# Kernel optimization log

Hardware: AMD Instinct MI355X
Metric: run time of the kernel (lower is better)

## Reference

```python
import jax, jax.numpy as jnp
import numpy as np

DIM = 512
K = 64          # num_clusters
GHOST = 1
ALPHA = 100.0
EPS = 1e-12


def _l2norm(v, axis):
    return v / jnp.maximum(jnp.linalg.norm(v, axis=axis, keepdims=True), EPS)


def setup_inputs() -> dict:
    key = jax.random.key(0)
    k_x, k_c = jax.random.split(key)
    x = jax.random.normal(k_x, (64, DIM, 32, 32), dtype=jnp.float32)
    # centroids ~ orthogonal init in torch; random normal rows, unit-ish scale
    centroids = jax.random.normal(k_c, (K + GHOST, DIM), dtype=jnp.float32) / np.sqrt(DIM)
    conv_w = 2.0 * ALPHA * centroids            # [K+g, C] (1x1 conv kernel squeezed)
    conv_b = -ALPHA * jnp.linalg.norm(centroids, axis=1)  # [K+g]
    return {"x": x, "centroids": centroids, "conv_w": conv_w, "conv_b": conv_b}


def reference(x, centroids, conv_w, conv_b):
    N, C, H, W = x.shape
    L = H * W
    # descriptor-wise L2 normalization over channel dim
    xn = _l2norm(x, axis=1)
    xf = xn.reshape(N, C, L)                                   # [N, C, L]
    # 1x1 conv == per-location matmul; softmax over clusters
    logits = jnp.einsum('kc,ncl->nkl', conv_w, xf) + conv_b[None, :, None]
    a = jax.nn.softmax(logits, axis=1)                         # [N, K+g, L]
    # vlad[n,k,c] = sum_l a[n,k,l]*(x[n,c,l]-cent[k,c])
    #            = (a @ x^T) - (sum_l a) * cent   -- avoids NxKxCxL tensor
    weighted = jnp.einsum('nkl,ncl->nkc', a, xf)               # [N, K+g, C]
    a_sum = jnp.sum(a, axis=-1)                                # [N, K+g]
    vlad = weighted - a_sum[:, :, None] * centroids[None]      # [N, K+g, C]
    vlad = vlad[:, :K, :]                                      # drop ghost clusters
    vlad = _l2norm(vlad, axis=2)                               # intra-normalization
    vlad = vlad.reshape(N, K * C)
    vlad = _l2norm(vlad, axis=1)                               # global L2
    return vlad
```

## Files before the change

### kernel.cpp

```cpp
#include <hip/hip_runtime.h>
#include <hip/hip_bf16.h>

#define C_DIM 512
#define L_DIM 1024
#define KK 64
#define KG 65
#define KP 80

using f32x4  = __attribute__((ext_vector_type(4))) float;
using bf16x8 = __attribute__((ext_vector_type(8))) short;

union U4 { uint4 u; bf16x8 b; };

__device__ __forceinline__ unsigned bfh(float x) { return __float_as_uint(x) >> 16; }
__device__ __forceinline__ float bfh_f(float x) { return __uint_as_float(__float_as_uint(x) & 0xFFFF0000u); }

__device__ __forceinline__ unsigned pack2(float a, float b) {
    return __builtin_amdgcn_perm(__float_as_uint(b), __float_as_uint(a), 0x07060302u);
}

__global__ void k_prep(const float* __restrict__ conv_w, const float* __restrict__ conv_b,
                       unsigned short* __restrict__ wpH, unsigned short* __restrict__ wpL,
                       float* __restrict__ wb)
{
    int ch = blockIdx.x;
    int kt = blockIdx.y;
    int t  = threadIdx.x;
    for (int p = 0; p < 2; ++p) {
        int idx = p * 256 + t;
        int lane = idx >> 3, j = idx & 7;
        int k = kt * 16 + (lane & 15);
        int c = ch * 32 + (lane >> 4) * 8 + j;
        float v = (k < KG) ? conv_w[k * C_DIM + c] : 0.f;
        unsigned h = bfh(v);
        float r = v - __uint_as_float(h << 16);
        int pos = ((ch * 5 + kt) << 9) + idx;
        wpH[pos] = (unsigned short)h;
        wpL[pos] = (unsigned short)bfh(r);
    }
    if (ch == 0 && kt == 0 && t < KP) wb[t] = (t < KG) ? conv_b[t] : -1e30f;
}

__global__ __launch_bounds__(256) void k_s1(
    const float* __restrict__ x, const unsigned short* __restrict__ wpH,
    const unsigned short* __restrict__ wpL, const float* __restrict__ wb,
    unsigned short* __restrict__ aPh, unsigned short* __restrict__ aPl,
    float* __restrict__ asum_part)
{
    const int lb = blockIdx.x, n = blockIdx.y;
    const int t = threadIdx.x, lane = t & 63, w = t >> 6;
    const int arow = lane & 15;
    const int agrp = lane >> 4;
    const int lw0 = lb * 128 + w * 32;

    const float* xbase = x + (size_t)n * C_DIM * L_DIM;

    f32x4 acc[5][2];
#pragma unroll
    for (int a = 0; a < 5; ++a)
#pragma unroll
        for (int b = 0; b < 2; ++b) acc[a][b] = (f32x4)0.f;
    float ss0 = 0.f, ss1 = 0.f;

    for (int ch = 0; ch < 16; ++ch) {
        const int c0 = ch * 32;
        float e0[8], e1[8];
#pragma unroll
        for (int j = 0; j < 8; ++j) {
            float2 v = *reinterpret_cast<const float2*>(
                &xbase[(size_t)(c0 + agrp * 8 + j) * L_DIM + lw0 + 2 * arow]);
            e0[j] = v.x;
            e1[j] = v.y;
        }
#pragma unroll
        for (int j = 0; j < 8; ++j) { ss0 += e0[j] * e0[j]; ss1 += e1[j] * e1[j]; }
        U4 bh[2], bl[2];
        bh[0].u.x = pack2(e0[0], e0[1]); bh[0].u.y = pack2(e0[2], e0[3]);
        bh[0].u.z = pack2(e0[4], e0[5]); bh[0].u.w = pack2(e0[6], e0[7]);
        bh[1].u.x = pack2(e1[0], e1[1]); bh[1].u.y = pack2(e1[2], e1[3]);
        bh[1].u.z = pack2(e1[4], e1[5]); bh[1].u.w = pack2(e1[6], e1[7]);
        float r0, r1, r2, r3;
        r0 = e0[0] - bfh_f(e0[0]); r1 = e0[1] - bfh_f(e0[1]);
        r2 = e0[2] - bfh_f(e0[2]); r3 = e0[3] - bfh_f(e0[3]);
        bl[0].u.x = pack2(r0, r1); bl[0].u.y = pack2(r2, r3);
        r0 = e0[4] - bfh_f(e0[4]); r1 = e0[5] - bfh_f(e0[5]);
        r2 = e0[6] - bfh_f(e0[6]); r3 = e0[7] - bfh_f(e0[7]);
        bl[0].u.z = pack2(r0, r1); bl[0].u.w = pack2(r2, r3);
        r0 = e1[0] - bfh_f(e1[0]); r1 = e1[1] - bfh_f(e1[1]);
        r2 = e1[2] - bfh_f(e1[2]); r3 = e1[3] - bfh_f(e1[3]);
        bl[1].u.x = pack2(r0, r1); bl[1].u.y = pack2(r2, r3);
        r0 = e1[4] - bfh_f(e1[4]); r1 = e1[5] - bfh_f(e1[5]);
        r2 = e1[6] - bfh_f(e1[6]); r3 = e1[7] - bfh_f(e1[7]);
        bl[1].u.z = pack2(r0, r1); bl[1].u.w = pack2(r2, r3);
        U4 ah[5], al[5];
#pragma unroll
        for (int kt = 0; kt < 5; ++kt) {
            int poff = (((ch * 5 + kt) << 6) + lane) << 3;
            ah[kt].u = *reinterpret_cast<const uint4*>(&wpH[poff]);
            al[kt].u = *reinterpret_cast<const uint4*>(&wpL[poff]);
        }
#pragma unroll
        for (int kt = 0; kt < 5; ++kt)
#pragma unroll
            for (int lt = 0; lt < 2; ++lt) {
                acc[kt][lt] = __builtin_amdgcn_mfma_f32_16x16x32_bf16(ah[kt].b, bh[lt].b, acc[kt][lt], 0, 0, 0);
                acc[kt][lt] = __builtin_amdgcn_mfma_f32_16x16x32_bf16(ah[kt].b, bl[lt].b, acc[kt][lt], 0, 0, 0);
                acc[kt][lt] = __builtin_amdgcn_mfma_f32_16x16x32_bf16(al[kt].b, bh[lt].b, acc[kt][lt], 0, 0, 0);
            }
    }

    ss0 += __shfl_xor(ss0, 16, 64); ss0 += __shfl_xor(ss0, 32, 64);
    ss1 += __shfl_xor(ss1, 16, 64); ss1 += __shfl_xor(ss1, 32, 64);
    float invc[2];
    invc[0] = 1.0f / fmaxf(sqrtf(ss0), 1e-12f);
    invc[1] = 1.0f / fmaxf(sqrtf(ss1), 1e-12f);

    float4 wbv[5];
#pragma unroll
    for (int kt = 0; kt < 5; ++kt)
        wbv[kt] = *reinterpret_cast<const float4*>(&wb[kt * 16 + agrp * 4]);

    float aval[5][2][4];
    float rs[2];
#pragma unroll
    for (int lt = 0; lt < 2; ++lt) {
        float m = -1e30f;
#pragma unroll
        for (int kt = 0; kt < 5; ++kt)
#pragma unroll
            for (int r = 0; r < 4; ++r) {
                float lg = acc[kt][lt][r] * invc[lt] + ((const float*)&wbv[kt])[r];
                aval[kt][lt][r] = lg;
                m = fmaxf(m, lg);
            }
        m = fmaxf(m, __shfl_xor(m, 16, 64));
        m = fmaxf(m, __shfl_xor(m, 32, 64));
        float s = 0.f;
#pragma unroll
        for (int kt = 0; kt < 5; ++kt)
#pragma unroll
            for (int r = 0; r < 4; ++r) {
                float e = __expf(aval[kt][lt][r] - m);
                aval[kt][lt][r] = e;
                s += e;
            }
        s += __shfl_xor(s, 16, 64);
        s += __shfl_xor(s, 32, 64);
        rs[lt] = 1.0f / s;
    }

#pragma unroll
    for (int kt = 0; kt < 4; ++kt)
#pragma unroll
        for (int r = 0; r < 4; ++r) {
            int k = kt * 16 + agrp * 4 + r;
            float s01 = 0.f;
#pragma unroll
            for (int lt = 0; lt < 2; ++lt) {
                float a = aval[kt][lt][r] * rs[lt];
                aval[kt][lt][r] = a;
                s01 += a;
            }
#pragma unroll
            for (int off = 8; off; off >>= 1) s01 += __shfl_xor(s01, off, 64);
            if ((lane & 15) == 0)
                asum_part[((n * 8 + lb) * 4 + w) * KK + k] = s01;
#pragma unroll
            for (int lt = 0; lt < 2; ++lt) {
                float ap = aval[kt][lt][r] * invc[lt];
                unsigned h = bfh(ap);
                float res = ap - __uint_as_float(h << 16);
                int idx = (n * KK + k) * L_DIM + lw0 + 2 * arow + lt;
                aPh[idx] = (unsigned short)h;
                aPl[idx] = (unsigned short)bfh(res);
            }
        }
}

#define S2P 72
__global__ __launch_bounds__(256) void k_s2(
    const float* __restrict__ x, const unsigned short* __restrict__ aPh,
    const unsigned short* __restrict__ aPl, float* __restrict__ weighted)
{
    __shared__ unsigned short Ah[64 * S2P], Al[64 * S2P];
    __shared__ unsigned short Bh[64 * S2P], Bl[64 * S2P];

    const int flat = blockIdx.x;
    const int cq = flat >> 6;
    const int n  = ((flat & 7) << 3) | ((flat >> 3) & 7);
    const int t = threadIdx.x, lane = t & 63, w = t >> 6;
    const int arow = lane & 15, agrp = lane >> 4;

    f32x4 acc[4];
#pragma unroll
    for (int a = 0; a < 4; ++a) acc[a] = (f32x4)0.f;

    for (int step = 0; step < 16; ++step) {
        const int l0 = step * 64;
        __syncthreads();
#pragma unroll
        for (int p = 0; p < 2; ++p) {
            int idx = p * 256 + t;
            int k = idx >> 3;
            int lc = (idx & 7) * 8;
            size_t g = (size_t)(n * KK + k) * L_DIM + l0 + lc;
            *reinterpret_cast<uint4*>(&Ah[k * S2P + lc]) = *reinterpret_cast<const uint4*>(&aPh[g]);
            *reinterpret_cast<uint4*>(&Al[k * S2P + lc]) = *reinterpret_cast<const uint4*>(&aPl[g]);
        }
#pragma unroll
        for (int p = 0; p < 4; ++p) {
            int idx = p * 256 + t;
            int c = idx >> 4;
            int lc = (idx & 15) * 4;
            float4 v = *reinterpret_cast<const float4*>(
                &x[((size_t)n * C_DIM + cq * 64 + c) * L_DIM + l0 + lc]);
            uint2 hw, lw;
            hw.x = pack2(v.x, v.y); hw.y = pack2(v.z, v.w);
            float r0 = v.x - bfh_f(v.x), r1 = v.y - bfh_f(v.y);
            float r2 = v.z - bfh_f(v.z), r3 = v.w - bfh_f(v.w);
            lw.x = pack2(r0, r1); lw.y = pack2(r2, r3);
            *reinterpret_cast<uint2*>(&Bh[c * S2P + lc]) = hw;
            *reinterpret_cast<uint2*>(&Bl[c * S2P + lc]) = lw;
        }
        __syncthreads();
#pragma unroll
        for (int ks = 0; ks < 2; ++ks) {
            const int koff = ks * 32 + agrp * 8;
            U4 bh, bl;
            bh.u = *reinterpret_cast<const uint4*>(&Bh[(w * 16 + arow) * S2P + koff]);
            bl.u = *reinterpret_cast<const uint4*>(&Bl[(w * 16 + arow) * S2P + koff]);
#pragma unroll
            for (int kt = 0; kt < 4; ++kt) {
                U4 ah, al;
                ah.u = *reinterpret_cast<const uint4*>(&Ah[(kt * 16 + arow) * S2P + koff]);
                al.u = *reinterpret_cast<const uint4*>(&Al[(kt * 16 + arow) * S2P + koff]);
                acc[kt] = __builtin_amdgcn_mfma_f32_16x16x32_bf16(ah.b, bh.b, acc[kt], 0, 0, 0);
                acc[kt] = __builtin_amdgcn_mfma_f32_16x16x32_bf16(ah.b, bl.b, acc[kt], 0, 0, 0);
                acc[kt] = __builtin_amdgcn_mfma_f32_16x16x32_bf16(al.b, bh.b, acc[kt], 0, 0, 0);
            }
        }
    }
#pragma unroll
    for (int kt = 0; kt < 4; ++kt)
#pragma unroll
        for (int r = 0; r < 4; ++r) {
            int k = kt * 16 + agrp * 4 + r;
            weighted[((size_t)n * KK + k) * C_DIM + cq * 64 + w * 16 + arow] = acc[kt][r];
        }
}

__global__ void k_rownorm(const float* __restrict__ weighted, const float* __restrict__ part,
                          const float* __restrict__ cent, float* __restrict__ a_sum,
                          float* __restrict__ rn)
{
    int nk = blockIdx.x;
    int n = nk >> 6, k = nk & 63;
    int t = threadIdx.x;
    float as = 0.f;
#pragma unroll
    for (int p = 0; p < 32; ++p) as += part[(n * 32 + p) * KK + k];
    if (t == 0) a_sum[nk] = as;
    float s = 0.f;
    for (int c = t; c < C_DIM; c += 256) {
        float v = weighted[(size_t)nk * C_DIM + c] - as * cent[k * C_DIM + c];
        s += v * v;
    }
#pragma unroll
    for (int off = 32; off; off >>= 1) s += __shfl_down(s, off, 64);
    __shared__ float red[4];
    if ((t & 63) == 0) red[t >> 6] = s;
    __syncthreads();
    if (t == 0) rn[nk] = red[0] + red[1] + red[2] + red[3];
}

__global__ void k_scale(const float* __restrict__ rn, float* __restrict__ scale)
{
    int n = blockIdx.x;
    int k = threadIdx.x;
    float s = rn[n * 64 + k];
    float nrm = sqrtf(s);
    float den = fmaxf(nrm, 1e-12f);
    float tk = nrm / den;
    float tot = tk * tk;
#pragma unroll
    for (int off = 32; off; off >>= 1) tot += __shfl_down(tot, off, 64);
    tot = __shfl(tot, 0, 64);
    float g = fmaxf(sqrtf(tot), 1e-12f);
    scale[n * 64 + k] = 1.0f / (den * g);
}

__global__ void k_out(const float* __restrict__ weighted, const float* __restrict__ a_sum,
                      const float* __restrict__ cent, const float* __restrict__ scale,
                      float* __restrict__ out)
{
    int nk = blockIdx.x;
    int k = nk & 63;
    int t = threadIdx.x;
    float as = a_sum[nk];
    float sc = scale[nk];
    for (int c = t; c < C_DIM; c += 256) {
        float v = weighted[(size_t)nk * C_DIM + c] - as * cent[k * C_DIM + c];
        out[(size_t)nk * C_DIM + c] = v * sc;
    }
}

extern "C" void kernel_launch(void* const* d_in, const int* in_sizes, int n_in,
                              void* d_out, int out_size, void* d_ws, size_t ws_size,
                              hipStream_t stream)
{
    const float* x    = (const float*)d_in[0];
    const float* cent = (const float*)d_in[1];
    const float* cw   = (const float*)d_in[2];
    const float* cb   = (const float*)d_in[3];
    float* out = (float*)d_out;
    char* ws = (char*)d_ws;

    unsigned short* wpH = (unsigned short*)(ws + 0);
    unsigned short* wpL = (unsigned short*)(ws + 131072);
    float*          wb  = (float*)(ws + 262144);
    unsigned short* aPh = (unsigned short*)(ws + 524288);
    unsigned short* aPl = (unsigned short*)(ws + 8912896);
    float* asum_part    = (float*)(ws + 17301504);
    float* a_sum        = (float*)(ws + 17825792);
    float* weighted     = (float*)(ws + 18874368);
    float* rn           = (float*)(ws + 35651584);
    float* scale        = (float*)(ws + 35667968);

    k_prep<<<dim3(16, 5), 256, 0, stream>>>(cw, cb, wpH, wpL, wb);
    k_s1<<<dim3(8, 64), 256, 0, stream>>>(x, wpH, wpL, wb, aPh, aPl, asum_part);
    k_s2<<<512, 256, 0, stream>>>(x, aPh, aPl, weighted);
    k_rownorm<<<4096, 256, 0, stream>>>(weighted, asum_part, cent, a_sum, rn);
    k_scale<<<64, 64, 0, stream>>>(rn, scale);
    k_out<<<4096, 256, 0, stream>>>(weighted, a_sum, cent, scale, out);
}
```

Before: 82.69 us.

## Fuse centroid subtraction and row-norm partials into s2 epilogue; pack a stores

The k_rownorm pass, which re-read the 8 MB weighted buffer, is removed. The s2 GEMM epilogue now subtracts a_sum*centroid, writes vlad, and emits per-block squared-norm partials that k_scale sums. A small k_asum kernel reduces the a_sum partials beforehand, and k_s1 packs its bf16 hi/lo pairs into 32-bit stores. The aim is to cut one full memory pass and the narrow 16-bit stores, in exchange for an extra tiny launch and more epilogue work in s2.

```diff
diff --git a/kernel.cpp b/kernel.cpp
--- a/kernel.cpp
+++ b/kernel.cpp
@@ -44,7 +44,7 @@
 __global__ __launch_bounds__(256) void k_s1(
     const float* __restrict__ x, const unsigned short* __restrict__ wpH,
     const unsigned short* __restrict__ wpL, const float* __restrict__ wb,
-    unsigned short* __restrict__ aPh, unsigned short* __restrict__ aPl,
+    unsigned* __restrict__ aPh32, unsigned* __restrict__ aPl32,
     float* __restrict__ asum_part)
 {
     const int lb = blockIdx.x, n = blockIdx.y;
@@ -165,25 +165,37 @@
             for (int off = 8; off; off >>= 1) s01 += __shfl_xor(s01, off, 64);
             if ((lane & 15) == 0)
                 asum_part[((n * 8 + lb) * 4 + w) * KK + k] = s01;
-#pragma unroll
-            for (int lt = 0; lt < 2; ++lt) {
-                float ap = aval[kt][lt][r] * invc[lt];
-                unsigned h = bfh(ap);
-                float res = ap - __uint_as_float(h << 16);
-                int idx = (n * KK + k) * L_DIM + lw0 + 2 * arow + lt;
-                aPh[idx] = (unsigned short)h;
-                aPl[idx] = (unsigned short)bfh(res);
-            }
-        }
+            float ap0 = aval[kt][0][r] * invc[0];
+            float ap1 = aval[kt][1][r] * invc[1];
+            unsigned h0 = bfh(ap0), h1 = bfh(ap1);
+            float q0 = ap0 - __uint_as_float(h0 << 16);
+            float q1 = ap1 - __uint_as_float(h1 << 16);
+            int widx = (n * KK + k) * (L_DIM / 2) + (lw0 >> 1) + arow;
+            aPh32[widx] = h0 | (h1 << 16);
+            aPl32[widx] = bfh(q0) | (bfh(q1) << 16);
+        }
+}
+
+__global__ void k_asum(const float* __restrict__ part, float* __restrict__ a_sum)
+{
+    int id = blockIdx.x * 256 + threadIdx.x;
+    int n = id >> 6, k = id & 63;
+    float s = 0.f;
+#pragma unroll
+    for (int p = 0; p < 32; ++p) s += part[(n * 32 + p) * KK + k];
+    a_sum[id] = s;
 }
 
 #define S2P 72
-__global__ __launch_bounds__(256) void k_s2(
+__global__ __launch_bounds__(256) void k_s2v(
     const float* __restrict__ x, const unsigned short* __restrict__ aPh,
-    const unsigned short* __restrict__ aPl, float* __restrict__ weighted)
+    const unsigned short* __restrict__ aPl, const float* __restrict__ a_sum,
+    const float* __restrict__ cent, float* __restrict__ vlad,
+    float* __restrict__ rnpart)
 {
     __shared__ unsigned short Ah[64 * S2P], Al[64 * S2P];
     __shared__ unsigned short Bh[64 * S2P], Bl[64 * S2P];
+    __shared__ float rnbuf[4][64];
 
     const int flat = blockIdx.x;
     const int cq = flat >> 6;
@@ -240,44 +252,45 @@
             }
         }
     }
+    const int c = cq * 64 + w * 16 + arow;
+    float myrn[4][4];
 #pragma unroll
     for (int kt = 0; kt < 4; ++kt)
 #pragma unroll
         for (int r = 0; r < 4; ++r) {
             int k = kt * 16 + agrp * 4 + r;
-            weighted[((size_t)n * KK + k) * C_DIM + cq * 64 + w * 16 + arow] = acc[kt][r];
-        }
-}
-
-__global__ void k_rownorm(const float* __restrict__ weighted, const float* __restrict__ part,
-                          const float* __restrict__ cent, float* __restrict__ a_sum,
-                          float* __restrict__ rn)
-{
-    int nk = blockIdx.x;
-    int n = nk >> 6, k = nk & 63;
-    int t = threadIdx.x;
-    float as = 0.f;
-#pragma unroll
-    for (int p = 0; p < 32; ++p) as += part[(n * 32 + p) * KK + k];
-    if (t == 0) a_sum[nk] = as;
-    float s = 0.f;
-    for (int c = t; c < C_DIM; c += 256) {
-        float v = weighted[(size_t)nk * C_DIM + c] - as * cent[k * C_DIM + c];
-        s += v * v;
-    }
-#pragma unroll
-    for (int off = 32; off; off >>= 1) s += __shfl_down(s, off, 64);
-    __shared__ float red[4];
-    if ((t & 63) == 0) red[t >> 6] = s;
+            float as = a_sum[n * 64 + k];
+            float cv = cent[k * C_DIM + c];
+            float v = acc[kt][r] - as * cv;
+            vlad[((size_t)n * KK + k) * C_DIM + c] = v;
+            float sq = v * v;
+            sq += __shfl_xor(sq, 1, 64);
+            sq += __shfl_xor(sq, 2, 64);
+            sq += __shfl_xor(sq, 4, 64);
+            sq += __shfl_xor(sq, 8, 64);
+            myrn[kt][r] = sq;
+        }
+    if (arow == 0) {
+#pragma unroll
+        for (int kt = 0; kt < 4; ++kt)
+#pragma unroll
+            for (int r = 0; r < 4; ++r)
+                rnbuf[w][kt * 16 + agrp * 4 + r] = myrn[kt][r];
+    }
     __syncthreads();
-    if (t == 0) rn[nk] = red[0] + red[1] + red[2] + red[3];
-}
-
-__global__ void k_scale(const float* __restrict__ rn, float* __restrict__ scale)
+    if (t < 64) {
+        float s = rnbuf[0][t] + rnbuf[1][t] + rnbuf[2][t] + rnbuf[3][t];
+        rnpart[((size_t)n * 64 + t) * 8 + cq] = s;
+    }
+}
+
+__global__ void k_scale(const float* __restrict__ rnpart, float* __restrict__ scale)
 {
     int n = blockIdx.x;
     int k = threadIdx.x;
-    float s = rn[n * 64 + k];
+    float s = 0.f;
+#pragma unroll
+    for (int q = 0; q < 8; ++q) s += rnpart[((size_t)n * 64 + k) * 8 + q];
     float nrm = sqrtf(s);
     float den = fmaxf(nrm, 1e-12f);
     float tk = nrm / den;
@@ -289,19 +302,14 @@
     scale[n * 64 + k] = 1.0f / (den * g);
 }
 
-__global__ void k_out(const float* __restrict__ weighted, const float* __restrict__ a_sum,
-                      const float* __restrict__ cent, const float* __restrict__ scale,
+__global__ void k_out(const float* __restrict__ vlad, const float* __restrict__ scale,
                       float* __restrict__ out)
 {
     int nk = blockIdx.x;
-    int k = nk & 63;
     int t = threadIdx.x;
-    float as = a_sum[nk];
     float sc = scale[nk];
-    for (int c = t; c < C_DIM; c += 256) {
-        float v = weighted[(size_t)nk * C_DIM + c] - as * cent[k * C_DIM + c];
-        out[(size_t)nk * C_DIM + c] = v * sc;
-    }
+    for (int c = t; c < C_DIM; c += 256)
+        out[(size_t)nk * C_DIM + c] = vlad[(size_t)nk * C_DIM + c] * sc;
 }
 
 extern "C" void kernel_launch(void* const* d_in, const int* in_sizes, int n_in,
@@ -322,14 +330,15 @@
     unsigned short* aPl = (unsigned short*)(ws + 8912896);
     float* asum_part    = (float*)(ws + 17301504);
     float* a_sum        = (float*)(ws + 17825792);
-    float* weighted     = (float*)(ws + 18874368);
-    float* rn           = (float*)(ws + 35651584);
-    float* scale        = (float*)(ws + 35667968);
+    float* vlad         = (float*)(ws + 18874368);
+    float* rnpart       = (float*)(ws + 27262976);
+    float* scale        = (float*)(ws + 27394048);
 
     k_prep<<<dim3(16, 5), 256, 0, stream>>>(cw, cb, wpH, wpL, wb);
-    k_s1<<<dim3(8, 64), 256, 0, stream>>>(x, wpH, wpL, wb, aPh, aPl, asum_part);
-    k_s2<<<512, 256, 0, stream>>>(x, aPh, aPl, weighted);
-    k_rownorm<<<4096, 256, 0, stream>>>(weighted, asum_part, cent, a_sum, rn);
-    k_scale<<<64, 64, 0, stream>>>(rn, scale);
-    k_out<<<4096, 256, 0, stream>>>(weighted, a_sum, cent, scale, out);
-}
+    k_s1<<<dim3(8, 64), 256, 0, stream>>>(x, wpH, wpL, wb,
+                                          (unsigned*)aPh, (unsigned*)aPl, asum_part);
+    k_asum<<<16, 256, 0, stream>>>(asum_part, a_sum);
+    k_s2v<<<512, 256, 0, stream>>>(x, aPh, aPl, a_sum, cent, vlad, rnpart);
+    k_scale<<<64, 64, 0, stream>>>(rnpart, scale);
+    k_out<<<4096, 256, 0, stream>>>(vlad, scale, out);
+}
```

After: 77.91 us. 1.06x faster.
